# Performance work log

Measured on AMD Instinct MI355X. Metric: run time of the kernel, lower is better.

Reference implementation:

```python
import jax, jax.numpy as jnp
import numpy as np

B, T, D = 32, 4096, 256
P, K, L = 2, 17, 3
NH, HD, FF, HID = 8, 32, 2048, 128


def _ln(x, w, b):
    m = x.mean(-1, keepdims=True)
    v = ((x - m) ** 2).mean(-1, keepdims=True)
    return (x - m) * jax.lax.rsqrt(v + 1e-5) * w + b


def _refine(x, w1, b1, w2, b2):
    # x: (B,P,K,D). Vectorized all-pairs: pair[b,p,i,j] = concat(x_i, x_j); MLP; mean over j; residual.
    xi = jnp.broadcast_to(x[:, :, :, None, :], (B, P, K, K, D))
    xj = jnp.broadcast_to(x[:, :, None, :, :], (B, P, K, K, D))
    pair = jnp.concatenate([xi, xj], axis=-1)  # (B,P,K,K,2D)
    h = jax.nn.relu(pair @ w1.T + b1)
    y = (h @ w2.T + b2).mean(axis=3)  # (B,P,K,D)
    return y + x


def _forward(memory, person_q, key_q, sa_in_w, sa_in_b, sa_out_w, sa_out_b,
             ca_in_w, ca_in_b, ca_out_w, ca_out_b, ff1_w, ff1_b, ff2_w, ff2_b,
             ln1_w, ln1_b, ln2_w, ln2_b, ln3_w, ln3_b,
             r1_w1, r1_b1, r1_w2, r1_b2, r2_w1, r2_b1, r2_w2, r2_b2, fc_w, fc_b):
    scale = 1.0 / np.sqrt(HD).astype(np.float32)
    # tgt for person p = person_q[p] + key_q, all persons vectorized into axis P
    x = jnp.broadcast_to(person_q[None, :, None, :] + key_q[None, None, :, :], (B, P, K, D))
    for l in range(L):
        # --- self-attention over K keypoint queries (post-norm TransformerDecoderLayer) ---
        qkv = x @ sa_in_w[l].T + sa_in_b[l]
        q, k, v = jnp.split(qkv, 3, axis=-1)
        qh = q.reshape(B, P, K, NH, HD)
        kh = k.reshape(B, P, K, NH, HD)
        vh = v.reshape(B, P, K, NH, HD)
        a = jax.nn.softmax(jnp.einsum('bpqhd,bpkhd->bphqk', qh, kh) * scale, axis=-1)
        o = jnp.einsum('bphqk,bpkhd->bpqhd', a, vh).reshape(B, P, K, D)
        x = _ln(x + o @ sa_out_w[l].T + sa_out_b[l], ln1_w[l], ln1_b[l])
        # --- cross-attention to memory; memory K/V computed once, shared across persons ---
        q = x @ ca_in_w[l][:D].T + ca_in_b[l][:D]
        mk = memory @ ca_in_w[l][D:2 * D].T + ca_in_b[l][D:2 * D]
        mv = memory @ ca_in_w[l][2 * D:].T + ca_in_b[l][2 * D:]
        qh = q.reshape(B, P, K, NH, HD)
        kh = mk.reshape(B, T, NH, HD)
        vh = mv.reshape(B, T, NH, HD)
        a = jax.nn.softmax(jnp.einsum('bpqhd,bthd->bphqt', qh, kh) * scale, axis=-1)
        o = jnp.einsum('bphqt,bthd->bpqhd', a, vh).reshape(B, P, K, D)
        x = _ln(x + o @ ca_out_w[l].T + ca_out_b[l], ln2_w[l], ln2_b[l])
        # --- feed-forward (ReLU, dim_feedforward=2048 default) ---
        h = jax.nn.relu(x @ ff1_w[l].T + ff1_b[l])
        x = _ln(x + h @ ff2_w[l].T + ff2_b[l], ln3_w[l], ln3_b[l])
    x = _refine(x, r1_w1, r1_b1, r1_w2, r1_b2)
    x = _refine(x, r2_w1, r2_b1, r2_w2, r2_b2)
    return x @ fc_w.T + fc_b  # (B, P, K, 3)


def setup_inputs() -> dict:
    key = jax.random.key(0)
    ks = iter(jax.random.split(key, 48))

    def w(shape, s=0.02):
        return jax.random.normal(next(ks), shape, dtype=jnp.float32) * s

    inp = {
        'memory': jax.random.normal(next(ks), (B, T, D), dtype=jnp.float32),
        'person_q': jax.random.normal(next(ks), (P, D), dtype=jnp.float32),
        'key_q': jax.random.normal(next(ks), (K, D), dtype=jnp.float32),
        'sa_in_w': w((L, 3 * D, D)), 'sa_in_b': jnp.zeros((L, 3 * D)),
        'sa_out_w': w((L, D, D)), 'sa_out_b': jnp.zeros((L, D)),
        'ca_in_w': w((L, 3 * D, D)), 'ca_in_b': jnp.zeros((L, 3 * D)),
        'ca_out_w': w((L, D, D)), 'ca_out_b': jnp.zeros((L, D)),
        'ff1_w': w((L, FF, D)), 'ff1_b': jnp.zeros((L, FF)),
        'ff2_w': w((L, D, FF)), 'ff2_b': jnp.zeros((L, D)),
        'ln1_w': jnp.ones((L, D)), 'ln1_b': jnp.zeros((L, D)),
        'ln2_w': jnp.ones((L, D)), 'ln2_b': jnp.zeros((L, D)),
        'ln3_w': jnp.ones((L, D)), 'ln3_b': jnp.zeros((L, D)),
        'r1_w1': w((HID, 2 * D)), 'r1_b1': jnp.zeros((HID,)),
        'r1_w2': w((D, HID)), 'r1_b2': jnp.zeros((D,)),
        'r2_w1': w((HID, 2 * D)), 'r2_b1': jnp.zeros((HID,)),
        'r2_w2': w((D, HID)), 'r2_b2': jnp.zeros((D,)),
        'fc_w': w((3, D)), 'fc_b': jnp.zeros((3,)),
    }
    return inp


def reference(memory, person_q, key_q, sa_in_w, sa_in_b, sa_out_w, sa_out_b,
              ca_in_w, ca_in_b, ca_out_w, ca_out_b, ff1_w, ff1_b, ff2_w, ff2_b,
              ln1_w, ln1_b, ln2_w, ln2_b, ln3_w, ln3_b,
              r1_w1, r1_b1, r1_w2, r1_b2, r2_w1, r2_b1, r2_w2, r2_b2, fc_w, fc_b):
    return _forward(memory, person_q, key_q, sa_in_w, sa_in_b, sa_out_w, sa_out_b,
                    ca_in_w, ca_in_b, ca_out_w, ca_out_b, ff1_w, ff1_b, ff2_w, ff2_b,
                    ln1_w, ln1_b, ln2_w, ln2_b, ln3_w, ln3_b,
                    r1_w1, r1_b1, r1_w2, r1_b2, r2_w1, r2_b1, r2_w2, r2_b2, fc_w, fc_b)
```

## Files before the change

kernel.cpp:

```cpp
#include <hip/hip_runtime.h>
#include <stdint.h>

#define NB   32
#define TSEQ 4096
#define DD   256
#define PP   2
#define KK   17
#define LL   3
#define NHH  8
#define HDD  32
#define FFD  2048
#define HIDD 128
#define ROWS 1088
#define SCALE 0.17677669529663689f

typedef __attribute__((ext_vector_type(4))) float f32x4;
typedef __attribute__((ext_vector_type(8))) short bf16x8;

static __device__ __forceinline__ unsigned cvtpk(float lo, float hi) {
  unsigned r;
  asm volatile("v_cvt_pk_bf16_f32 %0, %1, %2" : "=v"(r) : "v"(lo), "v"(hi));
  return r;
}
static __device__ __forceinline__ unsigned short f2bf(float f) {
  unsigned int x = __float_as_uint(f);
  return (unsigned short)((x + 0x7fffu + ((x >> 16) & 1u)) >> 16);
}
static __device__ __forceinline__ void gload_lds16(const void* g, void* l) {
  __builtin_amdgcn_global_load_lds(
      (const __attribute__((address_space(1))) unsigned int*)g,
      (__attribute__((address_space(3))) unsigned int*)l, 16, 0, 0);
}

__global__ __launch_bounds__(256) void cvt_bf16_kernel(
    const float* __restrict__ in, unsigned short* __restrict__ out, int n) {
  const int i = (blockIdx.x * 256 + threadIdx.x) * 8;
  if (i + 8 <= n) {
    const float4 f0 = *reinterpret_cast<const float4*>(in + i);
    const float4 f1 = *reinterpret_cast<const float4*>(in + i + 4);
    uint4 st;
    st.x = cvtpk(f0.x, f0.y); st.y = cvtpk(f0.z, f0.w);
    st.z = cvtpk(f1.x, f1.y); st.w = cvtpk(f1.z, f1.w);
    *reinterpret_cast<uint4*>(out + i) = st;
  }
}

__global__ __launch_bounds__(256) void init_x_kernel(
    const float* __restrict__ person_q, const float* __restrict__ key_q,
    float* __restrict__ x, unsigned short* __restrict__ x_bf) {
  const int row = blockIdx.x, tid = threadIdx.x;
  const int p = (row / KK) & 1, k = row % KK;
  const float v = person_q[p * DD + tid] + key_q[k * DD + tid];
  x[(size_t)row * DD + tid] = v;
  x_bf[(size_t)row * DD + tid] = f2bf(v);
}

__global__ __launch_bounds__(256) void gemm_kernel(
    const float* __restrict__ X, const float* __restrict__ W,
    const float* __restrict__ bias, const float* __restrict__ R,
    float* __restrict__ Y, int M, int N, int K, int wstride, int relu) {
  __shared__ float As[16][68];
  __shared__ float Bs[16][68];
  const int tid = threadIdx.x;
  const int m0 = blockIdx.y * 64, n0 = blockIdx.x * 64;
  const int tr = tid >> 4, tc = tid & 15;
  const int lr = tid >> 2, lk = (tid & 3) << 2;
  float acc[4][4] = {{0.f, 0.f, 0.f, 0.f}, {0.f, 0.f, 0.f, 0.f},
                     {0.f, 0.f, 0.f, 0.f}, {0.f, 0.f, 0.f, 0.f}};
  for (int k0 = 0; k0 < K; k0 += 16) {
    const float4 av = *reinterpret_cast<const float4*>(&X[(size_t)(m0 + lr) * K + k0 + lk]);
    int wn = n0 + lr; if (wn >= N) wn = N - 1;
    const float4 bv = *reinterpret_cast<const float4*>(&W[(size_t)wn * wstride + k0 + lk]);
    __syncthreads();
    As[lk + 0][lr] = av.x; As[lk + 1][lr] = av.y; As[lk + 2][lr] = av.z; As[lk + 3][lr] = av.w;
    Bs[lk + 0][lr] = bv.x; Bs[lk + 1][lr] = bv.y; Bs[lk + 2][lr] = bv.z; Bs[lk + 3][lr] = bv.w;
    __syncthreads();
#pragma unroll
    for (int kk = 0; kk < 16; ++kk) {
      const float4 a = *reinterpret_cast<const float4*>(&As[kk][tr << 2]);
      const float4 b = *reinterpret_cast<const float4*>(&Bs[kk][tc << 2]);
      const float aa[4] = {a.x, a.y, a.z, a.w};
      const float bb[4] = {b.x, b.y, b.z, b.w};
#pragma unroll
      for (int r = 0; r < 4; ++r)
#pragma unroll
        for (int c = 0; c < 4; ++c) acc[r][c] += aa[r] * bb[c];
    }
  }
#pragma unroll
  for (int r = 0; r < 4; ++r) {
    const int m = m0 + (tr << 2) + r;
#pragma unroll
    for (int c = 0; c < 4; ++c) {
      const int n = n0 + (tc << 2) + c;
      if (n < N) {
        float o = acc[r][c];
        if (bias) o += bias[n];
        if (relu) o = fmaxf(o, 0.f);
        if (R) o += R[(size_t)m * N + n];
        Y[(size_t)m * N + n] = o;
      }
    }
  }
}

__global__ __launch_bounds__(256) void gemm_bf16_kernel(
    const unsigned short* __restrict__ Xbf, const unsigned short* __restrict__ Wbf,
    const float* __restrict__ bias, const float* __restrict__ R,
    float* __restrict__ Yf, unsigned short* __restrict__ Ybf,
    int M, int N, int K, int wstride, int relu) {
  __shared__ unsigned short Xs[64 * 64];
  __shared__ unsigned short Ws[64 * 64];
  const int tid = threadIdx.x, lane = tid & 63, w = tid >> 6;
  const int g = lane >> 4, q16 = lane & 15;
  const int m0 = blockIdx.y * 64, n0 = blockIdx.x * 64;
  f32x4 acc[4];
#pragma unroll
  for (int nt = 0; nt < 4; ++nt) acc[nt] = (f32x4){0.f, 0.f, 0.f, 0.f};

  for (int k0 = 0; k0 < K; k0 += 64) {
    __syncthreads();
#pragma unroll
    for (int j = 0; j < 2; ++j) {
      const int cc = w * 2 + j;
      const int row = cc * 8 + (lane >> 3);
      const int sc = (lane & 7) ^ (row & 7);
      gload_lds16(Xbf + (size_t)(m0 + row) * K + k0 + sc * 8, &Xs[cc * 512]);
      gload_lds16(Wbf + (size_t)(n0 + row) * wstride + k0 + sc * 8, &Ws[cc * 512]);
    }
    asm volatile("s_waitcnt vmcnt(0)" ::: "memory");
    __syncthreads();
    const int arow = w * 16 + q16;
#pragma unroll
    for (int ks = 0; ks < 2; ++ks) {
      const bf16x8 a = *reinterpret_cast<const bf16x8*>(
          &Xs[arow * 64 + ((((ks << 2) + g) ^ (arow & 7)) << 3)]);
#pragma unroll
      for (int nt = 0; nt < 4; ++nt) {
        const int brow = nt * 16 + q16;
        const bf16x8 bfr = *reinterpret_cast<const bf16x8*>(
            &Ws[brow * 64 + ((((ks << 2) + g) ^ (brow & 7)) << 3)]);
        acc[nt] = __builtin_amdgcn_mfma_f32_16x16x32_bf16(a, bfr, acc[nt], 0, 0, 0);
      }
    }
  }
#pragma unroll
  for (int nt = 0; nt < 4; ++nt) {
    const int n = n0 + nt * 16 + q16;
    const float bv = bias ? bias[n] : 0.f;
#pragma unroll
    for (int r = 0; r < 4; ++r) {
      const int m = m0 + w * 16 + g * 4 + r;
      float o = acc[nt][r] + bv;
      if (relu) o = fmaxf(o, 0.f);
      if (R) o += R[(size_t)m * N + n];
      if (Yf) Yf[(size_t)m * N + n] = o;
      if (Ybf) Ybf[(size_t)m * N + n] = f2bf(o);
    }
  }
}

__global__ __launch_bounds__(64) void sa_attn_kernel(
    const float* __restrict__ qkv, unsigned short* __restrict__ attn_bf) {
  const int blk = blockIdx.x;
  const int h = blk & 7, bp = blk >> 3;
  const int rowbase = bp * KK;
  const int tid = threadIdx.x;
  __shared__ float qs[KK][36], ks[KK][36], vs[KK][36];
  __shared__ float ss[KK][20];
  __shared__ float lsum[KK];
  for (int i = tid; i < KK * HDD; i += 64) {
    const int r = i >> 5, d = i & 31;
    const size_t base = (size_t)(rowbase + r) * 768 + h * 32 + d;
    qs[r][d] = qkv[base];
    ks[r][d] = qkv[base + 256];
    vs[r][d] = qkv[base + 512];
  }
  __syncthreads();
  for (int i = tid; i < KK * KK; i += 64) {
    const int q = i / KK, k = i % KK;
    float s = 0.f;
#pragma unroll
    for (int d = 0; d < HDD; ++d) s += qs[q][d] * ks[k][d];
    ss[q][k] = s * SCALE;
  }
  __syncthreads();
  if (tid < KK) {
    float m = -1e30f;
    for (int k = 0; k < KK; ++k) m = fmaxf(m, ss[tid][k]);
    float l = 0.f;
    for (int k = 0; k < KK; ++k) { const float e = __expf(ss[tid][k] - m); ss[tid][k] = e; l += e; }
    lsum[tid] = l;
  }
  __syncthreads();
  for (int i = tid; i < KK * HDD; i += 64) {
    const int q = i >> 5, d = i & 31;
    float o = 0.f;
#pragma unroll
    for (int k = 0; k < KK; ++k) o += ss[q][k] * vs[k][d];
    attn_bf[(size_t)(rowbase + q) * DD + h * 32 + d] = f2bf(o / lsum[q]);
  }
}

__global__ __launch_bounds__(256) void wqk_kernel(
    const float* __restrict__ ca_in_w, unsigned short* __restrict__ Wqk_bf) {
  const int bx = blockIdx.x;
  const int l = bx >> 11, hc = bx & 2047;
  const int h = hc >> 8, c = hc & 255;
  const int d = threadIdx.x;
  const float* Wq = ca_in_w + (size_t)l * 196608 + (size_t)(h * 32) * 256;
  const float* Wk = ca_in_w + (size_t)l * 196608 + (size_t)(256 + h * 32) * 256;
  float acc = 0.f;
#pragma unroll
  for (int j = 0; j < 32; ++j) acc += Wk[(size_t)j * 256 + c] * Wq[(size_t)j * 256 + d];
  Wqk_bf[((size_t)l * 2048 + hc) * 256 + d] = f2bf(acc * SCALE);
}

__global__ __launch_bounds__(256) void bqk_kernel(
    const float* __restrict__ ca_in_w, const float* __restrict__ ca_in_b,
    float* __restrict__ bqk) {
  const int l = blockIdx.x >> 3, h = blockIdx.x & 7;
  const int c = threadIdx.x;
  const float* Wk = ca_in_w + (size_t)l * 196608 + (size_t)(256 + h * 32) * 256;
  const float* bq = ca_in_b + l * 768 + h * 32;
  float acc = 0.f;
#pragma unroll
  for (int j = 0; j < 32; ++j) acc += bq[j] * Wk[(size_t)j * 256 + c];
  bqk[(size_t)l * 2048 + h * 256 + c] = acc * SCALE;
}

__global__ __launch_bounds__(256) void prep_mem_kernel(
    const float* __restrict__ memory, unsigned short* __restrict__ mem_bf,
    unsigned short* __restrict__ memT) {
  const int b = blockIdx.x >> 6, tc = blockIdx.x & 63;
  const int tid = threadIdx.x;
  __shared__ unsigned short tile[64][264];
  for (int it = 0; it < 8; ++it) {
    const int idx = it * 256 + tid;
    const int t = idx >> 5, c8 = (idx & 31) << 3;
    const size_t goff = ((size_t)b * TSEQ + tc * 64 + t) * DD + c8;
    const float4 f0 = *reinterpret_cast<const float4*>(memory + goff);
    const float4 f1 = *reinterpret_cast<const float4*>(memory + goff + 4);
    uint4 st;
    st.x = cvtpk(f0.x, f0.y); st.y = cvtpk(f0.z, f0.w);
    st.z = cvtpk(f1.x, f1.y); st.w = cvtpk(f1.z, f1.w);
    *reinterpret_cast<uint4*>(&tile[t][c8]) = st;
    *reinterpret_cast<uint4*>(mem_bf + goff) = st;
  }
  __syncthreads();
  for (int it = 0; it < 8; ++it) {
    const int idx = it * 256 + tid;
    const int c = idx >> 3, t8 = (idx & 7) << 3;
    union { unsigned short v[8]; uint4 u; } pk;
#pragma unroll
    for (int j = 0; j < 8; ++j) pk.v[j] = tile[t8 + j][c];
    *reinterpret_cast<uint4*>(&memT[((size_t)b * DD + c) * TSEQ + tc * 64 + t8]) = pk.u;
  }
}

#define PS3 72
__global__ __launch_bounds__(256, 2) void ca_fused_kernel(
    const unsigned short* __restrict__ qkeff_bf, const unsigned short* __restrict__ mem_bf,
    const unsigned short* __restrict__ memT,
    float* __restrict__ o_part, float* __restrict__ m_part, float* __restrict__ l_part) {
  const int h = blockIdx.x >> 6;
  const int b = (blockIdx.x >> 1) & 31;
  const int half = blockIdx.x & 1;
  const int tid = threadIdx.x;
  const int lane = tid & 63, w = tid >> 6;
  const int g = lane >> 4, q16 = lane & 15;

  __shared__ unsigned short mem_lds[64 * 256];
  __shared__ unsigned short memT_lds[256 * 64];
  __shared__ unsigned short p_lds[48 * PS3];
  __shared__ float red_m[4 * 48];
  __shared__ float red_l[4 * 48];
  __shared__ float r_lds[48];

  bf16x8 bq[3][8];
#pragma unroll
  for (int qt = 0; qt < 3; ++qt) {
    const int ql = qt * 16 + q16;
    if (ql < 34) {
      const unsigned short* qbase = qkeff_bf + (size_t)(b * 34 + ql) * 2048 + h * 256;
#pragma unroll
      for (int ks = 0; ks < 8; ++ks)
        bq[qt][ks] = *reinterpret_cast<const bf16x8*>(qbase + ks * 32 + g * 8);
    } else {
#pragma unroll
      for (int ks = 0; ks < 8; ++ks) bq[qt][ks] = (bf16x8){0, 0, 0, 0, 0, 0, 0, 0};
    }
  }

  f32x4 ctx[3][4];
#pragma unroll
  for (int mt = 0; mt < 3; ++mt)
#pragma unroll
    for (int nt = 0; nt < 4; ++nt) ctx[mt][nt] = (f32x4){0.f, 0.f, 0.f, 0.f};
  float m_run[3] = {-1e30f, -1e30f, -1e30f};
  float l_run[3] = {0.f, 0.f, 0.f};

  const unsigned short* membb = mem_bf + (size_t)b * TSEQ * DD;
  const unsigned short* memTb = memT + (size_t)b * DD * TSEQ;

  for (int tile = 0; tile < 32; ++tile) {
    const int tbase = half * 2048 + tile * 64;
    __syncthreads();

#pragma unroll
    for (int j = 0; j < 8; ++j) {
      const int cc = w * 8 + j;
      const int trow = cc * 2 + (lane >> 5);
      const int sc = (lane & 31) ^ (trow & 7);
      gload_lds16(membb + (size_t)(tbase + trow) * DD + sc * 8, &mem_lds[cc * 512]);
    }
#pragma unroll
    for (int j = 0; j < 8; ++j) {
      const int cc = w * 8 + j;
      const int crow = cc * 8 + (lane >> 3);
      const int sc = (lane & 7) ^ (crow & 7);
      gload_lds16(memTb + (size_t)crow * TSEQ + tbase + sc * 8, &memT_lds[cc * 512]);
    }
    asm volatile("s_waitcnt vmcnt(0)" ::: "memory");
    __syncthreads();

    f32x4 sacc[3];
#pragma unroll
    for (int qt = 0; qt < 3; ++qt) sacc[qt] = (f32x4){0.f, 0.f, 0.f, 0.f};
    {
      const int arow = w * 16 + q16;
      __builtin_amdgcn_s_setprio(1);
#pragma unroll
      for (int ks = 0; ks < 8; ++ks) {
        const bf16x8 af = *reinterpret_cast<const bf16x8*>(
            &mem_lds[arow * 256 + ((((ks << 2) + g) ^ (arow & 7)) << 3)]);
#pragma unroll
        for (int qt = 0; qt < 3; ++qt)
          sacc[qt] = __builtin_amdgcn_mfma_f32_16x16x32_bf16(af, bq[qt][ks], sacc[qt], 0, 0, 0);
      }
      __builtin_amdgcn_s_setprio(0);
    }

#pragma unroll
    for (int qt = 0; qt < 3; ++qt) {
      float v = fmaxf(fmaxf(sacc[qt][0], sacc[qt][1]), fmaxf(sacc[qt][2], sacc[qt][3]));
      v = fmaxf(v, __shfl_xor(v, 16));
      v = fmaxf(v, __shfl_xor(v, 32));
      if (lane < 16) red_m[w * 48 + qt * 16 + lane] = v;
    }
    __syncthreads();

    float rfac[3], mnew[3];
#pragma unroll
    for (int qt = 0; qt < 3; ++qt) {
      const int q = qt * 16 + q16;
      const float tmax = fmaxf(fmaxf(red_m[q], red_m[48 + q]),
                               fmaxf(red_m[96 + q], red_m[144 + q]));
      mnew[qt] = fmaxf(m_run[qt], tmax);
      rfac[qt] = __expf(m_run[qt] - mnew[qt]);
      m_run[qt] = mnew[qt];
    }
    if (w == 0 && lane < 16) {
#pragma unroll
      for (int qt = 0; qt < 3; ++qt) r_lds[qt * 16 + lane] = rfac[qt];
    }

#pragma unroll
    for (int qt = 0; qt < 3; ++qt) {
      const float p0 = __expf(sacc[qt][0] - mnew[qt]);
      const float p1 = __expf(sacc[qt][1] - mnew[qt]);
      const float p2 = __expf(sacc[qt][2] - mnew[qt]);
      const float p3 = __expf(sacc[qt][3] - mnew[qt]);
      const int prow = (qt * 16 + q16) * PS3 + w * 16 + g * 4;
      *reinterpret_cast<unsigned*>(&p_lds[prow]) = cvtpk(p0, p1);
      *reinterpret_cast<unsigned*>(&p_lds[prow + 2]) = cvtpk(p2, p3);
      float ps = (p0 + p1) + (p2 + p3);
      ps += __shfl_xor(ps, 16);
      ps += __shfl_xor(ps, 32);
      if (lane < 16) red_l[w * 48 + qt * 16 + lane] = ps;
    }
    __syncthreads();

#pragma unroll
    for (int qt = 0; qt < 3; ++qt) {
      const int q = qt * 16 + q16;
      l_run[qt] = l_run[qt] * rfac[qt] +
                  ((red_l[q] + red_l[48 + q]) + (red_l[96 + q] + red_l[144 + q]));
    }
#pragma unroll
    for (int mt = 0; mt < 3; ++mt)
#pragma unroll
      for (int r = 0; r < 4; ++r) {
        const float rr = r_lds[mt * 16 + g * 4 + r];
#pragma unroll
        for (int nt = 0; nt < 4; ++nt) ctx[mt][nt][r] *= rr;
      }

    bf16x8 pf[3][2];
#pragma unroll
    for (int mt = 0; mt < 3; ++mt)
#pragma unroll
      for (int ks2 = 0; ks2 < 2; ++ks2)
        pf[mt][ks2] = *reinterpret_cast<const bf16x8*>(
            &p_lds[(mt * 16 + q16) * PS3 + ks2 * 32 + g * 8]);
    __builtin_amdgcn_s_setprio(1);
#pragma unroll
    for (int nt = 0; nt < 4; ++nt) {
      const int c = w * 64 + nt * 16 + q16;
#pragma unroll
      for (int ks2 = 0; ks2 < 2; ++ks2) {
        const bf16x8 bT = *reinterpret_cast<const bf16x8*>(
            &memT_lds[c * 64 + ((((ks2 << 2) + g) ^ (c & 7)) << 3)]);
#pragma unroll
        for (int mt = 0; mt < 3; ++mt)
          ctx[mt][nt] = __builtin_amdgcn_mfma_f32_16x16x32_bf16(pf[mt][ks2], bT,
                                                                ctx[mt][nt], 0, 0, 0);
      }
    }
    __builtin_amdgcn_s_setprio(0);
  }

#pragma unroll
  for (int mt = 0; mt < 3; ++mt)
#pragma unroll
    for (int r = 0; r < 4; ++r) {
      const int q = mt * 16 + g * 4 + r;
      if (q < 34) {
        const size_t orow = (size_t)(half * ROWS + b * 34 + q) * 2048;
#pragma unroll
        for (int nt = 0; nt < 4; ++nt)
          o_part[orow + h * 256 + w * 64 + nt * 16 + q16] = ctx[mt][nt][r];
      }
    }
  if (w == 0 && lane < 16) {
#pragma unroll
    for (int qt = 0; qt < 3; ++qt) {
      const int q = qt * 16 + lane;
      if (q < 34) {
        const size_t idx = (size_t)(half * ROWS + b * 34 + q) * 8 + h;
        m_part[idx] = m_run[qt];
        l_part[idx] = l_run[qt];
      }
    }
  }
}

__global__ __launch_bounds__(256) void ca_combine_kernel(
    const float* __restrict__ o_part, const float* __restrict__ m_part,
    const float* __restrict__ l_part, unsigned short* __restrict__ ctx_bf) {
  const int row = blockIdx.x, c = threadIdx.x;
#pragma unroll
  for (int h = 0; h < NHH; ++h) {
    const float m0 = m_part[(size_t)row * 8 + h];
    const float m1 = m_part[(size_t)(ROWS + row) * 8 + h];
    const float l0 = l_part[(size_t)row * 8 + h];
    const float l1 = l_part[(size_t)(ROWS + row) * 8 + h];
    const float M = fmaxf(m0, m1);
    const float w0 = __expf(m0 - M), w1 = __expf(m1 - M);
    const float denom = l0 * w0 + l1 * w1;
    const float o0 = o_part[(size_t)row * 2048 + h * 256 + c];
    const float o1 = o_part[(size_t)(ROWS + row) * 2048 + h * 256 + c];
    ctx_bf[(size_t)row * 2048 + h * 256 + c] = f2bf((o0 * w0 + o1 * w1) / denom);
  }
}

__global__ __launch_bounds__(256) void ln_kernel(
    const float* __restrict__ xin, const float* __restrict__ dlt,
    const float* __restrict__ w, const float* __restrict__ b,
    float* __restrict__ xout, unsigned short* __restrict__ xout_bf) {
  const int row = blockIdx.x, tid = threadIdx.x;
  const size_t base = (size_t)row * DD;
  const float v = xin[base + tid] + dlt[base + tid];
  float s = v, s2 = v * v;
#pragma unroll
  for (int off = 32; off > 0; off >>= 1) {
    s += __shfl_down(s, off);
    s2 += __shfl_down(s2, off);
  }
  __shared__ float ps[4], ps2[4];
  if ((tid & 63) == 0) { ps[tid >> 6] = s; ps2[tid >> 6] = s2; }
  __syncthreads();
  const float st = ps[0] + ps[1] + ps[2] + ps[3];
  const float st2 = ps2[0] + ps2[1] + ps2[2] + ps2[3];
  const float mean = st * (1.f / 256.f);
  const float var = st2 * (1.f / 256.f) - mean * mean;
  const float inv = rsqrtf(var + 1e-5f);
  const float o = (v - mean) * inv * w[tid] + b[tid];
  xout[base + tid] = o;
  xout_bf[base + tid] = f2bf(o);
}

__global__ __launch_bounds__(256) void wvo_kernel(
    const float* __restrict__ ca_in_w, const float* __restrict__ ca_out_w,
    unsigned short* __restrict__ Wvo_bf) {
  const int bx = blockIdx.x;
  const int h = bx & 7, dp = (bx >> 3) & 255, l = bx >> 11;
  const int c = threadIdx.x;
  const float* wout = ca_out_w + (size_t)l * 65536 + (size_t)dp * 256 + h * 32;
  const float* wv = ca_in_w + (size_t)l * 196608 + (size_t)(512 + h * 32) * 256 + c;
  float acc = 0.f;
#pragma unroll
  for (int j = 0; j < 32; ++j) acc += wout[j] * wv[(size_t)j * 256];
  Wvo_bf[((size_t)l * 256 + dp) * 2048 + h * 256 + c] = f2bf(acc);
}

__global__ __launch_bounds__(256) void bvo_kernel(
    const float* __restrict__ ca_out_w, const float* __restrict__ ca_in_b,
    const float* __restrict__ ca_out_b, float* __restrict__ bvo) {
  const int l = blockIdx.x, dp = threadIdx.x;
  float acc = ca_out_b[l * 256 + dp];
  for (int j = 0; j < 256; ++j)
    acc += ca_out_w[(size_t)l * 65536 + (size_t)dp * 256 + j] * ca_in_b[l * 768 + 512 + j];
  bvo[l * 256 + dp] = acc;
}

__global__ __launch_bounds__(256) void pairmean_kernel(
    const float* __restrict__ u, const float* __restrict__ v,
    unsigned short* __restrict__ hbar_bf) {
  const int bp = blockIdx.x, tid = threadIdx.x;
  const int r0 = bp * KK;
  __shared__ float us[KK][132], vs[KK][132];
  for (int i = tid; i < KK * HIDD; i += 256) {
    const int r = i >> 7, f = i & 127;
    us[r][f] = u[(size_t)(r0 + r) * HIDD + f];
    vs[r][f] = v[(size_t)(r0 + r) * HIDD + f];
  }
  __syncthreads();
  for (int i = tid; i < KK * HIDD; i += 256) {
    const int r = i >> 7, f = i & 127;
    float s = 0.f;
#pragma unroll
    for (int j = 0; j < KK; ++j) s += fmaxf(us[r][f] + vs[j][f], 0.f);
    hbar_bf[(size_t)(r0 + r) * HIDD + f] = f2bf(s * (1.0f / 17.0f));
  }
}

static void gemm(const float* X, const float* W, const float* bias, const float* R,
                 float* Y, int M, int N, int K, int wstride, int relu, hipStream_t s) {
  dim3 g((N + 63) / 64, M / 64);
  gemm_kernel<<<g, 256, 0, s>>>(X, W, bias, R, Y, M, N, K, wstride, relu);
}
static void gemm_bf(const unsigned short* X, const unsigned short* W, const float* bias,
                    const float* R, float* Yf, unsigned short* Ybf, int M, int N, int K,
                    int wstride, int relu, hipStream_t s) {
  dim3 g(N / 64, M / 64);
  gemm_bf16_kernel<<<g, 256, 0, s>>>(X, W, bias, R, Yf, Ybf, M, N, K, wstride, relu);
}
static void cvt(const float* in, unsigned short* out, size_t n, hipStream_t s) {
  cvt_bf16_kernel<<<(unsigned)((n / 8 + 255) / 256), 256, 0, s>>>(in, out, (int)n);
}

extern "C" void kernel_launch(void* const* d_in, const int* in_sizes, int n_in,
                              void* d_out, int out_size, void* d_ws, size_t ws_size,
                              hipStream_t stream) {
  const float* memory   = (const float*)d_in[0];
  const float* person_q = (const float*)d_in[1];
  const float* key_q    = (const float*)d_in[2];
  const float* sa_in_w  = (const float*)d_in[3];
  const float* sa_in_b  = (const float*)d_in[4];
  const float* sa_out_w = (const float*)d_in[5];
  const float* sa_out_b = (const float*)d_in[6];
  const float* ca_in_w  = (const float*)d_in[7];
  const float* ca_in_b  = (const float*)d_in[8];
  const float* ca_out_w = (const float*)d_in[9];
  const float* ca_out_b = (const float*)d_in[10];
  const float* ff1_w = (const float*)d_in[11];
  const float* ff1_b = (const float*)d_in[12];
  const float* ff2_w = (const float*)d_in[13];
  const float* ff2_b = (const float*)d_in[14];
  const float* ln1_w = (const float*)d_in[15];
  const float* ln1_b = (const float*)d_in[16];
  const float* ln2_w = (const float*)d_in[17];
  const float* ln2_b = (const float*)d_in[18];
  const float* ln3_w = (const float*)d_in[19];
  const float* ln3_b = (const float*)d_in[20];
  const float* r1_w1 = (const float*)d_in[21];
  const float* r1_b1 = (const float*)d_in[22];
  const float* r1_w2 = (const float*)d_in[23];
  const float* r1_b2 = (const float*)d_in[24];
  const float* r2_w1 = (const float*)d_in[25];
  const float* r2_b1 = (const float*)d_in[26];
  const float* r2_w2 = (const float*)d_in[27];
  const float* r2_b2 = (const float*)d_in[28];
  const float* fc_w  = (const float*)d_in[29];
  const float* fc_b  = (const float*)d_in[30];
  float* out = (float*)d_out;

  char* wsb = (char*)d_ws;
  size_t off = 0;
  auto alloc = [&](size_t bytes) -> char* {
    char* p = wsb + off;
    off += (bytes + 255) & ~(size_t)255;
    return p;
  };
  float* x      = (float*)alloc((size_t)ROWS * DD * 4);
  float* qkv    = (float*)alloc((size_t)ROWS * 768 * 4);
  float* delta  = (float*)alloc((size_t)ROWS * DD * 4);
  float* bvo    = (float*)alloc(3 * 256 * 4);
  float* bqk    = (float*)alloc((size_t)3 * 2048 * 4);
  float* ubuf   = (float*)alloc((size_t)ROWS * HIDD * 4);
  float* vbuf   = (float*)alloc((size_t)ROWS * HIDD * 4);
  float* o_part = (float*)alloc((size_t)2 * ROWS * 2048 * 4);
  float* m_part = (float*)alloc((size_t)2 * ROWS * 8 * 4);
  float* l_part = (float*)alloc((size_t)2 * ROWS * 8 * 4);
  unsigned short* x_bf     = (unsigned short*)alloc((size_t)ROWS * DD * 2);
  unsigned short* attn_bf  = (unsigned short*)alloc((size_t)ROWS * DD * 2);
  unsigned short* hff_bf   = (unsigned short*)alloc((size_t)ROWS * 2048 * 2);
  unsigned short* ctx_bf   = (unsigned short*)alloc((size_t)ROWS * 2048 * 2);
  unsigned short* qkeff_bf = (unsigned short*)alloc((size_t)ROWS * 2048 * 2);
  unsigned short* hbar_bf  = (unsigned short*)alloc((size_t)ROWS * HIDD * 2);
  unsigned short* mem_bf   = (unsigned short*)alloc((size_t)NB * TSEQ * DD * 2);
  unsigned short* memT     = (unsigned short*)alloc((size_t)NB * TSEQ * DD * 2);
  unsigned short* sa_in_bf  = (unsigned short*)alloc((size_t)3 * 768 * 256 * 2);
  unsigned short* sa_out_bf = (unsigned short*)alloc((size_t)3 * 256 * 256 * 2);
  unsigned short* Wqk_bf   = (unsigned short*)alloc((size_t)3 * 2048 * 256 * 2);
  unsigned short* ff1_bf   = (unsigned short*)alloc((size_t)3 * 2048 * 256 * 2);
  unsigned short* ff2_bf   = (unsigned short*)alloc((size_t)3 * 256 * 2048 * 2);
  unsigned short* Wvo_bf   = (unsigned short*)alloc((size_t)3 * 256 * 2048 * 2);
  unsigned short* r1w1_bf  = (unsigned short*)alloc((size_t)HIDD * 512 * 2);
  unsigned short* r1w2_bf  = (unsigned short*)alloc((size_t)DD * HIDD * 2);
  unsigned short* r2w1_bf  = (unsigned short*)alloc((size_t)HIDD * 512 * 2);
  unsigned short* r2w2_bf  = (unsigned short*)alloc((size_t)DD * HIDD * 2);

  prep_mem_kernel<<<NB * 64, 256, 0, stream>>>(memory, mem_bf, memT);
  cvt(sa_in_w, sa_in_bf, (size_t)3 * 768 * 256, stream);
  cvt(sa_out_w, sa_out_bf, (size_t)3 * 256 * 256, stream);
  cvt(ff1_w, ff1_bf, (size_t)3 * 2048 * 256, stream);
  cvt(ff2_w, ff2_bf, (size_t)3 * 256 * 2048, stream);
  cvt(r1_w1, r1w1_bf, (size_t)HIDD * 512, stream);
  cvt(r1_w2, r1w2_bf, (size_t)DD * HIDD, stream);
  cvt(r2_w1, r2w1_bf, (size_t)HIDD * 512, stream);
  cvt(r2_w2, r2w2_bf, (size_t)DD * HIDD, stream);
  wqk_kernel<<<6144, 256, 0, stream>>>(ca_in_w, Wqk_bf);
  bqk_kernel<<<24, 256, 0, stream>>>(ca_in_w, ca_in_b, bqk);
  wvo_kernel<<<6144, 256, 0, stream>>>(ca_in_w, ca_out_w, Wvo_bf);
  bvo_kernel<<<3, 256, 0, stream>>>(ca_out_w, ca_in_b, ca_out_b, bvo);
  init_x_kernel<<<ROWS, 256, 0, stream>>>(person_q, key_q, x, x_bf);

  for (int l = 0; l < LL; ++l) {
    gemm_bf(x_bf, sa_in_bf + (size_t)l * 768 * 256, sa_in_b + l * 768, nullptr,
            qkv, nullptr, ROWS, 768, 256, 256, 0, stream);
    sa_attn_kernel<<<512, 64, 0, stream>>>(qkv, attn_bf);
    gemm_bf(attn_bf, sa_out_bf + (size_t)l * 256 * 256, sa_out_b + l * 256, nullptr,
            delta, nullptr, ROWS, 256, 256, 256, 0, stream);
    ln_kernel<<<ROWS, 256, 0, stream>>>(x, delta, ln1_w + l * 256, ln1_b + l * 256, x, x_bf);
    gemm_bf(x_bf, Wqk_bf + (size_t)l * 2048 * 256, bqk + l * 2048, nullptr,
            nullptr, qkeff_bf, ROWS, 2048, 256, 256, 0, stream);
    ca_fused_kernel<<<512, 256, 0, stream>>>(qkeff_bf, mem_bf, memT, o_part, m_part, l_part);
    ca_combine_kernel<<<ROWS, 256, 0, stream>>>(o_part, m_part, l_part, ctx_bf);
    gemm_bf(ctx_bf, Wvo_bf + (size_t)l * 256 * 2048, bvo + l * 256, nullptr,
            delta, nullptr, ROWS, 256, 2048, 2048, 0, stream);
    ln_kernel<<<ROWS, 256, 0, stream>>>(x, delta, ln2_w + l * 256, ln2_b + l * 256, x, x_bf);
    gemm_bf(x_bf, ff1_bf + (size_t)l * 2048 * 256, ff1_b + l * 2048, nullptr,
            nullptr, hff_bf, ROWS, 2048, 256, 256, 1, stream);
    gemm_bf(hff_bf, ff2_bf + (size_t)l * 256 * 2048, ff2_b + l * 256, nullptr,
            delta, nullptr, ROWS, 256, 2048, 2048, 0, stream);
    ln_kernel<<<ROWS, 256, 0, stream>>>(x, delta, ln3_w + l * 256, ln3_b + l * 256, x, x_bf);
  }

  const unsigned short* rw1_bf[2] = {r1w1_bf, r2w1_bf};
  const unsigned short* rw2_bf[2] = {r1w2_bf, r2w2_bf};
  const float* rb1[2] = {r1_b1, r2_b1};
  const float* rb2[2] = {r1_b2, r2_b2};
  for (int r = 0; r < 2; ++r) {
    gemm_bf(x_bf, rw1_bf[r], rb1[r], nullptr, ubuf, nullptr,
            ROWS, 128, 256, 512, 0, stream);
    gemm_bf(x_bf, rw1_bf[r] + 256, nullptr, nullptr, vbuf, nullptr,
            ROWS, 128, 256, 512, 0, stream);
    pairmean_kernel<<<64, 256, 0, stream>>>(ubuf, vbuf, hbar_bf);
    gemm_bf(hbar_bf, rw2_bf[r], rb2[r], x, x, x_bf,
            ROWS, 256, 128, 128, 0, stream);
  }

  gemm(x, fc_w, fc_b, nullptr, out, ROWS, 3, 256, 256, 0, stream);
}
```

Measured before the change: 777.7 us.

## Restructure cross-attention kernel with double-buffered tiles and per-wave independent softmax

The fused cross-attention kernel now runs one 512-thread block per (head, batch) instead of two 256-thread blocks split over the sequence. Each block double-buffers memory tiles so the next tile's global-to-LDS load overlaps the current tile's compute. Each pair of waves keeps its own online-softmax state over a 16-row slice of each tile, which removes the cross-wave LDS max/sum reductions and two barriers per tile. The P·V product is fed straight from registers with a 16x16x16 MFMA instead of a round trip through LDS. In exchange the combine step merges four partial results instead of two, the partial buffers grow, there are half as many blocks, and the per-thread accumulator count doubles. The eight weight-conversion launches are also merged into one multi-job kernel.

Result: slower. 979.2 us (+25.9%).

```diff
diff --git a/kernel.cpp b/kernel.cpp
--- a/kernel.cpp
+++ b/kernel.cpp
@@ -16,6 +16,7 @@
 
 typedef __attribute__((ext_vector_type(4))) float f32x4;
 typedef __attribute__((ext_vector_type(8))) short bf16x8;
+typedef __attribute__((ext_vector_type(4))) short bf16x4;
 
 static __device__ __forceinline__ unsigned cvtpk(float lo, float hi) {
   unsigned r;
@@ -32,16 +33,22 @@
       (__attribute__((address_space(3))) unsigned int*)l, 16, 0, 0);
 }
 
-__global__ __launch_bounds__(256) void cvt_bf16_kernel(
-    const float* __restrict__ in, unsigned short* __restrict__ out, int n) {
-  const int i = (blockIdx.x * 256 + threadIdx.x) * 8;
-  if (i + 8 <= n) {
-    const float4 f0 = *reinterpret_cast<const float4*>(in + i);
-    const float4 f1 = *reinterpret_cast<const float4*>(in + i + 4);
-    uint4 st;
-    st.x = cvtpk(f0.x, f0.y); st.y = cvtpk(f0.z, f0.w);
-    st.z = cvtpk(f1.x, f1.y); st.w = cvtpk(f1.z, f1.w);
-    *reinterpret_cast<uint4*>(out + i) = st;
+struct CvtJob { const float* src; unsigned short* dst; int n; };
+struct CvtJobs8 { CvtJob j[8]; };
+__global__ __launch_bounds__(256) void cvt_multi_kernel(CvtJobs8 jobs) {
+#pragma unroll
+  for (int jj = 0; jj < 8; ++jj) {
+    const float* src = jobs.j[jj].src;
+    unsigned short* dst = jobs.j[jj].dst;
+    const int n8 = jobs.j[jj].n >> 3;
+    for (int i = blockIdx.x * 256 + threadIdx.x; i < n8; i += gridDim.x * 256) {
+      const float4 f0 = *reinterpret_cast<const float4*>(src + i * 8);
+      const float4 f1 = *reinterpret_cast<const float4*>(src + i * 8 + 4);
+      uint4 st;
+      st.x = cvtpk(f0.x, f0.y); st.y = cvtpk(f0.z, f0.w);
+      st.z = cvtpk(f1.x, f1.y); st.w = cvtpk(f1.z, f1.w);
+      *reinterpret_cast<uint4*>(dst + i * 8) = st;
+    }
   }
 }
 
@@ -258,24 +265,19 @@
   }
 }
 
-#define PS3 72
-__global__ __launch_bounds__(256, 2) void ca_fused_kernel(
+__global__ __launch_bounds__(512, 2) void ca_fused_kernel(
     const unsigned short* __restrict__ qkeff_bf, const unsigned short* __restrict__ mem_bf,
     const unsigned short* __restrict__ memT,
     float* __restrict__ o_part, float* __restrict__ m_part, float* __restrict__ l_part) {
-  const int h = blockIdx.x >> 6;
-  const int b = (blockIdx.x >> 1) & 31;
-  const int half = blockIdx.x & 1;
+  const int h = blockIdx.x >> 5;
+  const int b = blockIdx.x & 31;
   const int tid = threadIdx.x;
   const int lane = tid & 63, w = tid >> 6;
+  const int tg = w >> 1, cg = w & 1;
   const int g = lane >> 4, q16 = lane & 15;
 
-  __shared__ unsigned short mem_lds[64 * 256];
-  __shared__ unsigned short memT_lds[256 * 64];
-  __shared__ unsigned short p_lds[48 * PS3];
-  __shared__ float red_m[4 * 48];
-  __shared__ float red_l[4 * 48];
-  __shared__ float r_lds[48];
+  __shared__ unsigned short mem_lds[2][64 * 256];
+  __shared__ unsigned short memT_lds[2][256 * 64];
 
   bf16x8 bq[3][8];
 #pragma unroll
@@ -291,153 +293,126 @@
       for (int ks = 0; ks < 8; ++ks) bq[qt][ks] = (bf16x8){0, 0, 0, 0, 0, 0, 0, 0};
     }
   }
-
-  f32x4 ctx[3][4];
-#pragma unroll
-  for (int mt = 0; mt < 3; ++mt)
-#pragma unroll
-    for (int nt = 0; nt < 4; ++nt) ctx[mt][nt] = (f32x4){0.f, 0.f, 0.f, 0.f};
+  asm volatile("s_waitcnt vmcnt(0)" ::: "memory");
+
+  f32x4 ctx[3][8];
+#pragma unroll
+  for (int qt = 0; qt < 3; ++qt)
+#pragma unroll
+    for (int cm = 0; cm < 8; ++cm) ctx[qt][cm] = (f32x4){0.f, 0.f, 0.f, 0.f};
   float m_run[3] = {-1e30f, -1e30f, -1e30f};
   float l_run[3] = {0.f, 0.f, 0.f};
 
   const unsigned short* membb = mem_bf + (size_t)b * TSEQ * DD;
   const unsigned short* memTb = memT + (size_t)b * DD * TSEQ;
 
-  for (int tile = 0; tile < 32; ++tile) {
-    const int tbase = half * 2048 + tile * 64;
-    __syncthreads();
-
-#pragma unroll
-    for (int j = 0; j < 8; ++j) {
-      const int cc = w * 8 + j;
+  auto stage_tile = [&](int tile, int buf) {
+    const int tbase = tile * 64;
+#pragma unroll
+    for (int j = 0; j < 4; ++j) {
+      const int cc = w * 4 + j;
       const int trow = cc * 2 + (lane >> 5);
       const int sc = (lane & 31) ^ (trow & 7);
-      gload_lds16(membb + (size_t)(tbase + trow) * DD + sc * 8, &mem_lds[cc * 512]);
-    }
-#pragma unroll
-    for (int j = 0; j < 8; ++j) {
-      const int cc = w * 8 + j;
+      gload_lds16(membb + (size_t)(tbase + trow) * DD + sc * 8, &mem_lds[buf][cc * 512]);
+    }
+#pragma unroll
+    for (int j = 0; j < 4; ++j) {
+      const int cc = w * 4 + j;
       const int crow = cc * 8 + (lane >> 3);
       const int sc = (lane & 7) ^ (crow & 7);
-      gload_lds16(memTb + (size_t)crow * TSEQ + tbase + sc * 8, &memT_lds[cc * 512]);
-    }
-    asm volatile("s_waitcnt vmcnt(0)" ::: "memory");
+      gload_lds16(memTb + (size_t)crow * TSEQ + tbase + sc * 8, &memT_lds[buf][cc * 512]);
+    }
+  };
+
+  stage_tile(0, 0);
+  for (int tile = 0; tile < 64; ++tile) {
+    const int buf = tile & 1;
+    if (tile + 1 < 64) {
+      stage_tile(tile + 1, buf ^ 1);
+      asm volatile("s_waitcnt vmcnt(8)" ::: "memory");
+    } else {
+      asm volatile("s_waitcnt vmcnt(0)" ::: "memory");
+    }
     __syncthreads();
 
     f32x4 sacc[3];
 #pragma unroll
     for (int qt = 0; qt < 3; ++qt) sacc[qt] = (f32x4){0.f, 0.f, 0.f, 0.f};
     {
-      const int arow = w * 16 + q16;
-      __builtin_amdgcn_s_setprio(1);
+      const int arow = tg * 16 + q16;
 #pragma unroll
       for (int ks = 0; ks < 8; ++ks) {
         const bf16x8 af = *reinterpret_cast<const bf16x8*>(
-            &mem_lds[arow * 256 + ((((ks << 2) + g) ^ (arow & 7)) << 3)]);
+            &mem_lds[buf][arow * 256 + ((((ks << 2) + g) ^ (arow & 7)) << 3)]);
 #pragma unroll
         for (int qt = 0; qt < 3; ++qt)
           sacc[qt] = __builtin_amdgcn_mfma_f32_16x16x32_bf16(af, bq[qt][ks], sacc[qt], 0, 0, 0);
       }
-      __builtin_amdgcn_s_setprio(0);
-    }
-
+    }
+
+    float rfac[3];
+    bf16x4 pb[3];
 #pragma unroll
     for (int qt = 0; qt < 3; ++qt) {
       float v = fmaxf(fmaxf(sacc[qt][0], sacc[qt][1]), fmaxf(sacc[qt][2], sacc[qt][3]));
       v = fmaxf(v, __shfl_xor(v, 16));
       v = fmaxf(v, __shfl_xor(v, 32));
-      if (lane < 16) red_m[w * 48 + qt * 16 + lane] = v;
-    }
-    __syncthreads();
-
-    float rfac[3], mnew[3];
-#pragma unroll
-    for (int qt = 0; qt < 3; ++qt) {
-      const int q = qt * 16 + q16;
-      const float tmax = fmaxf(fmaxf(red_m[q], red_m[48 + q]),
-                               fmaxf(red_m[96 + q], red_m[144 + q]));
-      mnew[qt] = fmaxf(m_run[qt], tmax);
-      rfac[qt] = __expf(m_run[qt] - mnew[qt]);
-      m_run[qt] = mnew[qt];
-    }
-    if (w == 0 && lane < 16) {
-#pragma unroll
-      for (int qt = 0; qt < 3; ++qt) r_lds[qt * 16 + lane] = rfac[qt];
-    }
-
-#pragma unroll
-    for (int qt = 0; qt < 3; ++qt) {
-      const float p0 = __expf(sacc[qt][0] - mnew[qt]);
-      const float p1 = __expf(sacc[qt][1] - mnew[qt]);
-      const float p2 = __expf(sacc[qt][2] - mnew[qt]);
-      const float p3 = __expf(sacc[qt][3] - mnew[qt]);
-      const int prow = (qt * 16 + q16) * PS3 + w * 16 + g * 4;
-      *reinterpret_cast<unsigned*>(&p_lds[prow]) = cvtpk(p0, p1);
-      *reinterpret_cast<unsigned*>(&p_lds[prow + 2]) = cvtpk(p2, p3);
+      const float mnew = fmaxf(m_run[qt], v);
+      rfac[qt] = __expf(m_run[qt] - mnew);
+      m_run[qt] = mnew;
+      const float p0 = __expf(sacc[qt][0] - mnew);
+      const float p1 = __expf(sacc[qt][1] - mnew);
+      const float p2 = __expf(sacc[qt][2] - mnew);
+      const float p3 = __expf(sacc[qt][3] - mnew);
       float ps = (p0 + p1) + (p2 + p3);
       ps += __shfl_xor(ps, 16);
       ps += __shfl_xor(ps, 32);
-      if (lane < 16) red_l[w * 48 + qt * 16 + lane] = ps;
+      l_run[qt] = l_run[qt] * rfac[qt] + ps;
+      union { bf16x4 v4; unsigned u[2]; } pk;
+      pk.u[0] = cvtpk(p0, p1);
+      pk.u[1] = cvtpk(p2, p3);
+      pb[qt] = pk.v4;
+    }
+#pragma unroll
+    for (int qt = 0; qt < 3; ++qt)
+#pragma unroll
+      for (int cm = 0; cm < 8; ++cm) ctx[qt][cm] *= rfac[qt];
+
+    asm volatile("s_nop 2");
+    {
+      const int chunkb = 2 * tg + (g >> 1);
+      const int sub4 = (g & 1) * 4;
+#pragma unroll
+      for (int cm = 0; cm < 8; ++cm) {
+        const int crow = cg * 128 + cm * 16 + q16;
+        const bf16x4 av = *reinterpret_cast<const bf16x4*>(
+            &memT_lds[buf][crow * 64 + ((chunkb ^ (crow & 7)) << 3) + sub4]);
+#pragma unroll
+        for (int qt = 0; qt < 3; ++qt)
+          asm volatile("v_mfma_f32_16x16x16_bf16 %0, %1, %2, %0"
+                       : "+v"(ctx[qt][cm]) : "v"(av), "v"(pb[qt]));
+      }
     }
     __syncthreads();
-
-#pragma unroll
-    for (int qt = 0; qt < 3; ++qt) {
-      const int q = qt * 16 + q16;
-      l_run[qt] = l_run[qt] * rfac[qt] +
-                  ((red_l[q] + red_l[48 + q]) + (red_l[96 + q] + red_l[144 + q]));
-    }
-#pragma unroll
-    for (int mt = 0; mt < 3; ++mt)
-#pragma unroll
-      for (int r = 0; r < 4; ++r) {
-        const float rr = r_lds[mt * 16 + g * 4 + r];
-#pragma unroll
-        for (int nt = 0; nt < 4; ++nt) ctx[mt][nt][r] *= rr;
-      }
-
-    bf16x8 pf[3][2];
-#pragma unroll
-    for (int mt = 0; mt < 3; ++mt)
-#pragma unroll
-      for (int ks2 = 0; ks2 < 2; ++ks2)
-        pf[mt][ks2] = *reinterpret_cast<const bf16x8*>(
-            &p_lds[(mt * 16 + q16) * PS3 + ks2 * 32 + g * 8]);
-    __builtin_amdgcn_s_setprio(1);
-#pragma unroll
-    for (int nt = 0; nt < 4; ++nt) {
-      const int c = w * 64 + nt * 16 + q16;
-#pragma unroll
-      for (int ks2 = 0; ks2 < 2; ++ks2) {
-        const bf16x8 bT = *reinterpret_cast<const bf16x8*>(
-            &memT_lds[c * 64 + ((((ks2 << 2) + g) ^ (c & 7)) << 3)]);
-#pragma unroll
-        for (int mt = 0; mt < 3; ++mt)
-          ctx[mt][nt] = __builtin_amdgcn_mfma_f32_16x16x32_bf16(pf[mt][ks2], bT,
-                                                                ctx[mt][nt], 0, 0, 0);
-      }
-    }
-    __builtin_amdgcn_s_setprio(0);
-  }
-
-#pragma unroll
-  for (int mt = 0; mt < 3; ++mt)
-#pragma unroll
-    for (int r = 0; r < 4; ++r) {
-      const int q = mt * 16 + g * 4 + r;
-      if (q < 34) {
-        const size_t orow = (size_t)(half * ROWS + b * 34 + q) * 2048;
-#pragma unroll
-        for (int nt = 0; nt < 4; ++nt)
-          o_part[orow + h * 256 + w * 64 + nt * 16 + q16] = ctx[mt][nt][r];
-      }
-    }
-  if (w == 0 && lane < 16) {
+  }
+
+#pragma unroll
+  for (int qt = 0; qt < 3; ++qt) {
+    const int q = qt * 16 + q16;
+    if (q < 34) {
+      const size_t orow = (size_t)(tg * ROWS + b * 34 + q) * 2048 + h * 256 + cg * 128;
+#pragma unroll
+      for (int cm = 0; cm < 8; ++cm)
+        *reinterpret_cast<float4*>(&o_part[orow + cm * 16 + g * 4]) =
+            (float4){ctx[qt][cm][0], ctx[qt][cm][1], ctx[qt][cm][2], ctx[qt][cm][3]};
+    }
+  }
+  if (cg == 0 && lane < 16) {
 #pragma unroll
     for (int qt = 0; qt < 3; ++qt) {
       const int q = qt * 16 + lane;
       if (q < 34) {
-        const size_t idx = (size_t)(half * ROWS + b * 34 + q) * 8 + h;
+        const size_t idx = (size_t)(tg * ROWS + b * 34 + q) * 8 + h;
         m_part[idx] = m_run[qt];
         l_part[idx] = l_run[qt];
       }
@@ -451,16 +426,21 @@
   const int row = blockIdx.x, c = threadIdx.x;
 #pragma unroll
   for (int h = 0; h < NHH; ++h) {
-    const float m0 = m_part[(size_t)row * 8 + h];
-    const float m1 = m_part[(size_t)(ROWS + row) * 8 + h];
-    const float l0 = l_part[(size_t)row * 8 + h];
-    const float l1 = l_part[(size_t)(ROWS + row) * 8 + h];
-    const float M = fmaxf(m0, m1);
-    const float w0 = __expf(m0 - M), w1 = __expf(m1 - M);
-    const float denom = l0 * w0 + l1 * w1;
-    const float o0 = o_part[(size_t)row * 2048 + h * 256 + c];
-    const float o1 = o_part[(size_t)(ROWS + row) * 2048 + h * 256 + c];
-    ctx_bf[(size_t)row * 2048 + h * 256 + c] = f2bf((o0 * w0 + o1 * w1) / denom);
+    float m[4], l[4];
+#pragma unroll
+    for (int p = 0; p < 4; ++p) {
+      m[p] = m_part[(size_t)(p * ROWS + row) * 8 + h];
+      l[p] = l_part[(size_t)(p * ROWS + row) * 8 + h];
+    }
+    const float M = fmaxf(fmaxf(m[0], m[1]), fmaxf(m[2], m[3]));
+    float wgt[4], denom = 0.f;
+#pragma unroll
+    for (int p = 0; p < 4; ++p) { wgt[p] = __expf(m[p] - M); denom += l[p] * wgt[p]; }
+    float o = 0.f;
+#pragma unroll
+    for (int p = 0; p < 4; ++p)
+      o += o_part[(size_t)(p * ROWS + row) * 2048 + h * 256 + c] * wgt[p];
+    ctx_bf[(size_t)row * 2048 + h * 256 + c] = f2bf(o / denom);
   }
 }
 
@@ -545,9 +525,6 @@
                     int wstride, int relu, hipStream_t s) {
   dim3 g(N / 64, M / 64);
   gemm_bf16_kernel<<<g, 256, 0, s>>>(X, W, bias, R, Yf, Ybf, M, N, K, wstride, relu);
-}
-static void cvt(const float* in, unsigned short* out, size_t n, hipStream_t s) {
-  cvt_bf16_kernel<<<(unsigned)((n / 8 + 255) / 256), 256, 0, s>>>(in, out, (int)n);
 }
 
 extern "C" void kernel_launch(void* const* d_in, const int* in_sizes, int n_in,
@@ -600,9 +577,9 @@
   float* bqk    = (float*)alloc((size_t)3 * 2048 * 4);
   float* ubuf   = (float*)alloc((size_t)ROWS * HIDD * 4);
   float* vbuf   = (float*)alloc((size_t)ROWS * HIDD * 4);
-  float* o_part = (float*)alloc((size_t)2 * ROWS * 2048 * 4);
-  float* m_part = (float*)alloc((size_t)2 * ROWS * 8 * 4);
-  float* l_part = (float*)alloc((size_t)2 * ROWS * 8 * 4);
+  float* o_part = (float*)alloc((size_t)4 * ROWS * 2048 * 4);
+  float* m_part = (float*)alloc((size_t)4 * ROWS * 8 * 4);
+  float* l_part = (float*)alloc((size_t)4 * ROWS * 8 * 4);
   unsigned short* x_bf     = (unsigned short*)alloc((size_t)ROWS * DD * 2);
   unsigned short* attn_bf  = (unsigned short*)alloc((size_t)ROWS * DD * 2);
   unsigned short* hff_bf   = (unsigned short*)alloc((size_t)ROWS * 2048 * 2);
@@ -623,14 +600,16 @@
   unsigned short* r2w2_bf  = (unsigned short*)alloc((size_t)DD * HIDD * 2);
 
   prep_mem_kernel<<<NB * 64, 256, 0, stream>>>(memory, mem_bf, memT);
-  cvt(sa_in_w, sa_in_bf, (size_t)3 * 768 * 256, stream);
-  cvt(sa_out_w, sa_out_bf, (size_t)3 * 256 * 256, stream);
-  cvt(ff1_w, ff1_bf, (size_t)3 * 2048 * 256, stream);
-  cvt(ff2_w, ff2_bf, (size_t)3 * 256 * 2048, stream);
-  cvt(r1_w1, r1w1_bf, (size_t)HIDD * 512, stream);
-  cvt(r1_w2, r1w2_bf, (size_t)DD * HIDD, stream);
-  cvt(r2_w1, r2w1_bf, (size_t)HIDD * 512, stream);
-  cvt(r2_w2, r2w2_bf, (size_t)DD * HIDD, stream);
+  CvtJobs8 jobs;
+  jobs.j[0] = {sa_in_w,  sa_in_bf,  3 * 768 * 256};
+  jobs.j[1] = {sa_out_w, sa_out_bf, 3 * 256 * 256};
+  jobs.j[2] = {ff1_w,    ff1_bf,    3 * 2048 * 256};
+  jobs.j[3] = {ff2_w,    ff2_bf,    3 * 256 * 2048};
+  jobs.j[4] = {r1_w1,    r1w1_bf,   HIDD * 512};
+  jobs.j[5] = {r1_w2,    r1w2_bf,   DD * HIDD};
+  jobs.j[6] = {r2_w1,    r2w1_bf,   HIDD * 512};
+  jobs.j[7] = {r2_w2,    r2w2_bf,   DD * HIDD};
+  cvt_multi_kernel<<<1024, 256, 0, stream>>>(jobs);
   wqk_kernel<<<6144, 256, 0, stream>>>(ca_in_w, Wqk_bf);
   bqk_kernel<<<24, 256, 0, stream>>>(ca_in_w, ca_in_b, bqk);
   wvo_kernel<<<6144, 256, 0, stream>>>(ca_in_w, ca_out_w, Wvo_bf);
@@ -646,7 +625,7 @@
     ln_kernel<<<ROWS, 256, 0, stream>>>(x, delta, ln1_w + l * 256, ln1_b + l * 256, x, x_bf);
     gemm_bf(x_bf, Wqk_bf + (size_t)l * 2048 * 256, bqk + l * 2048, nullptr,
             nullptr, qkeff_bf, ROWS, 2048, 256, 256, 0, stream);
-    ca_fused_kernel<<<512, 256, 0, stream>>>(qkeff_bf, mem_bf, memT, o_part, m_part, l_part);
+    ca_fused_kernel<<<256, 512, 0, stream>>>(qkeff_bf, mem_bf, memT, o_part, m_part, l_part);
     ca_combine_kernel<<<ROWS, 256, 0, stream>>>(o_part, m_part, l_part, ctx_bf);
     gemm_bf(ctx_bf, Wvo_bf + (size_t)l * 256 * 2048, bvo + l * 256, nullptr,
             delta, nullptr, ROWS, 256, 2048, 2048, 0, stream);
```
